# Performance work log

Measured on AMD Instinct MI355X. Metric: run time of the kernel, lower is better.

## Reference

```python
import jax, jax.numpy as jnp
import numpy as np

LN2 = float(np.log(2.0))
N_ATOMS = 100_000
N_PAIRS = 2_000_000
F = 64     # number_of_atom_features
R = 16     # number_of_radial_basis_functions
N_RES = 3


def setup_inputs() -> dict:
    key = jax.random.key(0)
    ks = jax.random.split(key, 16)
    s = 0.05
    inp = {
        "pair_indices": jax.random.randint(ks[0], (2, N_PAIRS), 0, N_ATOMS, dtype=jnp.int32),
        "f_ij": jax.random.normal(ks[1], (N_PAIRS, 1, R), dtype=jnp.float32),
        "d_ij": jax.random.uniform(ks[2], (N_PAIRS, 1), dtype=jnp.float32),
        "atomic_embedding": jax.random.normal(ks[3], (N_ATOMS, F), dtype=jnp.float32),
        # AttentionMask parameter G: [F, R]
        "G": jax.random.normal(ks[4], (F, R), dtype=jnp.float32),
        # interaction_i / interaction_j linear layers (stored as [in, out])
        "Wi": jax.random.normal(ks[5], (F, F), dtype=jnp.float32) * s,
        "bi": jnp.zeros((F,), dtype=jnp.float32),
        "Wj": jax.random.normal(ks[6], (F, F), dtype=jnp.float32) * s,
        "bj": jnp.zeros((F,), dtype=jnp.float32),
        # residual blocks, stacked over N_RES
        "res_W1": jax.random.normal(ks[7], (N_RES, F, F), dtype=jnp.float32) * s,
        "res_b1": jnp.zeros((N_RES, F), dtype=jnp.float32),
        "res_W2": jax.random.normal(ks[8], (N_RES, F, F), dtype=jnp.float32) * s,
        "res_b2": jnp.zeros((N_RES, F), dtype=jnp.float32),
        # process_v linear
        "Wv": jax.random.normal(ks[9], (F, F), dtype=jnp.float32) * s,
        "bv": jnp.zeros((F,), dtype=jnp.float32),
    }
    return inp


def reference(pair_indices, f_ij, d_ij, atomic_embedding,
              G, Wi, bi, Wj, bj, res_W1, res_b1, res_W2, res_b2, Wv, bv):
    idx_i, idx_j = pair_indices[0], pair_indices[1]
    f = f_ij.squeeze(1)                                  # [P, R]

    # ShiftedSoftplus on node embeddings
    x = jax.nn.softplus(atomic_embedding) - LN2          # [N, F]

    x_i_prime = jax.nn.softplus(x @ Wi + bi)             # [N, F]
    x_j_prime = jax.nn.softplus(x[idx_j] @ Wj + bj)      # [P, F] (gather)
    f_prime = f @ G.T                                    # [P, F] attention mask

    msg = x_j_prime * f_prime                            # [P, F]
    summed = jax.ops.segment_sum(msg, idx_i, num_segments=atomic_embedding.shape[0])

    v = x_i_prime + summed                               # [N, F]
    for l in range(res_W1.shape[0]):
        h = jax.nn.softplus(v @ res_W1[l] + res_b1[l])
        v = v + (h @ res_W2[l] + res_b2[l])
    return jax.nn.softplus(v) @ Wv + bv
```

## Files before the change

kernel.cpp:

```cpp
#include <hip/hip_runtime.h>
#include <math.h>

#define FDIM 64
#define RDIM 16
#define LN2F 0.69314718055994530942f
#define LTS 68

typedef __bf16 bf8_t __attribute__((ext_vector_type(8)));
typedef float  f4_t  __attribute__((ext_vector_type(4)));

__device__ __forceinline__ float sp(float x) {
    return fmaxf(x, 0.0f) + __logf(1.0f + __expf(-fabsf(x)));
}

__global__ __launch_bounds__(256) void k_prep(
    const float* s0, const float* s1, const float* s2, const float* s3,
    const float* s4, const float* s5, const float* s6, const float* s7,
    const float* s8, __bf16* __restrict__ dst)
{
    const float* srcs[9] = {s0, s1, s2, s3, s4, s5, s6, s7, s8};
    const float* W = srcs[blockIdx.x];
    __bf16* d = dst + (size_t)blockIdx.x * 4096;
    for (int slot = threadIdx.x; slot < 512; slot += 256) {
        int f = slot >> 6, l = slot & 63;
        int kt = f >> 2, nt = f & 3;
        int row0 = kt * 32 + (l >> 4) * 8;
        int col = nt * 16 + (l & 15);
#pragma unroll
        for (int j = 0; j < 8; ++j)
            d[slot * 8 + j] = (__bf16)W[(row0 + j) * FDIM + col];
    }
}

__global__ __launch_bounds__(256) void k_hist(
    const int* __restrict__ idx_i, int* __restrict__ cnt, int P)
{
    int t = blockIdx.x * blockDim.x + threadIdx.x;
    int n = gridDim.x * blockDim.x;
    for (int p = t; p < P; p += n) atomicAdd(&cnt[idx_i[p]], 1);
}

__device__ __forceinline__ void tile_in(float* T, const float* __restrict__ src,
                                        int a0, int rows, int lane)
{
#pragma unroll 4
    for (int i = 0; i < 16; ++i) {
        int r = i * 4 + (lane >> 4);
        int col = (lane & 15) * 4;
        float4 val = make_float4(0.f, 0.f, 0.f, 0.f);
        if (r < rows) val = *(const float4*)&src[(size_t)(a0 + r) * FDIM + col];
        *(float4*)&T[r * LTS + col] = val;
    }
}

__device__ __forceinline__ void build_a(const float* T, int lane, bool actLn2,
                                        bf8_t (&aF)[4][2])
{
    const int l15 = lane & 15, quad = lane >> 4;
#pragma unroll
    for (int mt = 0; mt < 4; ++mt) {
#pragma unroll
        for (int kt = 0; kt < 2; ++kt) {
            const float* rp = &T[(mt * 16 + l15) * LTS + kt * 32 + quad * 8];
            float4 u0 = *(const float4*)rp;
            float4 u1 = *(const float4*)(rp + 4);
            float e[8] = {u0.x, u0.y, u0.z, u0.w, u1.x, u1.y, u1.z, u1.w};
            bf8_t f;
#pragma unroll
            for (int j = 0; j < 8; ++j) {
                float t = actLn2 ? (sp(e[j]) - LN2F) : e[j];
                f[j] = (__bf16)t;
            }
            aF[mt][kt] = f;
        }
    }
}

__global__ __launch_bounds__(256) void k_atoms(
    const float* __restrict__ emb, const __bf16* __restrict__ wf,
    const float* __restrict__ bi, const float* __restrict__ bj,
    float* __restrict__ v, float* __restrict__ y, int N)
{
    __shared__ float tile[4][64 * LTS];
    const int lane = threadIdx.x & 63;
    const int wv = threadIdx.x >> 6;
    float* T = tile[wv];
    const int l15 = lane & 15, quad = lane >> 4;

    const bf8_t* wiF = (const bf8_t*)wf;
    const bf8_t* wjF = (const bf8_t*)(wf + 4096);
    bf8_t wi[2][4], wj[2][4];
#pragma unroll
    for (int kt = 0; kt < 2; ++kt)
#pragma unroll
        for (int nt = 0; nt < 4; ++nt) {
            wi[kt][nt] = wiF[(kt * 4 + nt) * 64 + lane];
            wj[kt][nt] = wjF[(kt * 4 + nt) * 64 + lane];
        }
    float biv[4], bjv[4];
#pragma unroll
    for (int nt = 0; nt < 4; ++nt) {
        biv[nt] = bi[nt * 16 + l15];
        bjv[nt] = bj[nt * 16 + l15];
    }

    const int nTiles = (N + 63) >> 6;
    for (int t = blockIdx.x * 4 + wv; t < nTiles; t += gridDim.x * 4) {
        const int a0 = t << 6;
        const int rows = min(64, N - a0);
        tile_in(T, emb, a0, rows, lane);
        bf8_t aF[4][2];
        build_a(T, lane, true, aF);
#pragma unroll
        for (int mt = 0; mt < 4; ++mt)
#pragma unroll
            for (int nt = 0; nt < 4; ++nt) {
                f4_t acc = {biv[nt], biv[nt], biv[nt], biv[nt]};
                acc = __builtin_amdgcn_mfma_f32_16x16x32_bf16(aF[mt][0], wi[0][nt], acc, 0, 0, 0);
                acc = __builtin_amdgcn_mfma_f32_16x16x32_bf16(aF[mt][1], wi[1][nt], acc, 0, 0, 0);
#pragma unroll
                for (int reg = 0; reg < 4; ++reg) {
                    int r = mt * 16 + quad * 4 + reg;
                    if (r < rows) v[(size_t)(a0 + r) * FDIM + nt * 16 + l15] = sp(acc[reg]);
                }
            }
#pragma unroll
        for (int mt = 0; mt < 4; ++mt)
#pragma unroll
            for (int nt = 0; nt < 4; ++nt) {
                f4_t acc = {bjv[nt], bjv[nt], bjv[nt], bjv[nt]};
                acc = __builtin_amdgcn_mfma_f32_16x16x32_bf16(aF[mt][0], wj[0][nt], acc, 0, 0, 0);
                acc = __builtin_amdgcn_mfma_f32_16x16x32_bf16(aF[mt][1], wj[1][nt], acc, 0, 0, 0);
#pragma unroll
                for (int reg = 0; reg < 4; ++reg) {
                    int r = mt * 16 + quad * 4 + reg;
                    if (r < rows) y[(size_t)(a0 + r) * FDIM + nt * 16 + l15] = sp(acc[reg]);
                }
            }
    }
}

__global__ __launch_bounds__(256) void k_post(
    const __bf16* __restrict__ wf,
    const float* __restrict__ rb1, const float* __restrict__ rb2,
    const float* __restrict__ bv,
    float* __restrict__ v, int N)
{
    __shared__ float tile[4][64 * LTS];
    const int lane = threadIdx.x & 63;
    const int wv = threadIdx.x >> 6;
    float* T = tile[wv];
    const int l15 = lane & 15, quad = lane >> 4;

    float b1v[3][4], b2v[3][4], bvv[4];
#pragma unroll
    for (int l = 0; l < 3; ++l)
#pragma unroll
        for (int nt = 0; nt < 4; ++nt) {
            b1v[l][nt] = rb1[l * FDIM + nt * 16 + l15];
            b2v[l][nt] = rb2[l * FDIM + nt * 16 + l15];
        }
#pragma unroll
    for (int nt = 0; nt < 4; ++nt) bvv[nt] = bv[nt * 16 + l15];

    const int nTiles = (N + 63) >> 6;
    for (int t = blockIdx.x * 4 + wv; t < nTiles; t += gridDim.x * 4) {
        const int a0 = t << 6;
        const int rows = min(64, N - a0);
        tile_in(T, v, a0, rows, lane);
        float vC[16][4];
#pragma unroll
        for (int mt = 0; mt < 4; ++mt)
#pragma unroll
            for (int nt = 0; nt < 4; ++nt)
#pragma unroll
                for (int reg = 0; reg < 4; ++reg)
                    vC[mt * 4 + nt][reg] =
                        T[(mt * 16 + quad * 4 + reg) * LTS + nt * 16 + l15];

        for (int l = 0; l < 3; ++l) {
            const bf8_t* w1f = (const bf8_t*)(wf + (size_t)(2 * l) * 4096);
            const bf8_t* w2f = (const bf8_t*)(wf + (size_t)(2 * l + 1) * 4096);
            bf8_t aF[4][2];
            build_a(T, lane, false, aF);
#pragma unroll
            for (int mt = 0; mt < 4; ++mt)
#pragma unroll
                for (int nt = 0; nt < 4; ++nt) {
                    f4_t acc = {b1v[l][nt], b1v[l][nt], b1v[l][nt], b1v[l][nt]};
                    acc = __builtin_amdgcn_mfma_f32_16x16x32_bf16(aF[mt][0], w1f[(0 * 4 + nt) * 64 + lane], acc, 0, 0, 0);
                    acc = __builtin_amdgcn_mfma_f32_16x16x32_bf16(aF[mt][1], w1f[(1 * 4 + nt) * 64 + lane], acc, 0, 0, 0);
#pragma unroll
                    for (int reg = 0; reg < 4; ++reg)
                        T[(mt * 16 + quad * 4 + reg) * LTS + nt * 16 + l15] = sp(acc[reg]);
                }
            bf8_t hF[4][2];
            build_a(T, lane, false, hF);
#pragma unroll
            for (int mt = 0; mt < 4; ++mt)
#pragma unroll
                for (int nt = 0; nt < 4; ++nt) {
                    f4_t acc = {b2v[l][nt], b2v[l][nt], b2v[l][nt], b2v[l][nt]};
                    acc = __builtin_amdgcn_mfma_f32_16x16x32_bf16(hF[mt][0], w2f[(0 * 4 + nt) * 64 + lane], acc, 0, 0, 0);
                    acc = __builtin_amdgcn_mfma_f32_16x16x32_bf16(hF[mt][1], w2f[(1 * 4 + nt) * 64 + lane], acc, 0, 0, 0);
#pragma unroll
                    for (int reg = 0; reg < 4; ++reg)
                        vC[mt * 4 + nt][reg] += acc[reg];
                }
            if (l < 2) {
#pragma unroll
                for (int mt = 0; mt < 4; ++mt)
#pragma unroll
                    for (int nt = 0; nt < 4; ++nt)
#pragma unroll
                        for (int reg = 0; reg < 4; ++reg)
                            T[(mt * 16 + quad * 4 + reg) * LTS + nt * 16 + l15] =
                                vC[mt * 4 + nt][reg];
            }
        }
#pragma unroll
        for (int mt = 0; mt < 4; ++mt)
#pragma unroll
            for (int nt = 0; nt < 4; ++nt)
#pragma unroll
                for (int reg = 0; reg < 4; ++reg)
                    T[(mt * 16 + quad * 4 + reg) * LTS + nt * 16 + l15] =
                        sp(vC[mt * 4 + nt][reg]);
        bf8_t fF[4][2];
        build_a(T, lane, false, fF);
        const bf8_t* wvf = (const bf8_t*)(wf + (size_t)6 * 4096);
#pragma unroll
        for (int mt = 0; mt < 4; ++mt)
#pragma unroll
            for (int nt = 0; nt < 4; ++nt) {
                f4_t acc = {bvv[nt], bvv[nt], bvv[nt], bvv[nt]};
                acc = __builtin_amdgcn_mfma_f32_16x16x32_bf16(fF[mt][0], wvf[(0 * 4 + nt) * 64 + lane], acc, 0, 0, 0);
                acc = __builtin_amdgcn_mfma_f32_16x16x32_bf16(fF[mt][1], wvf[(1 * 4 + nt) * 64 + lane], acc, 0, 0, 0);
#pragma unroll
                for (int reg = 0; reg < 4; ++reg) {
                    int r = mt * 16 + quad * 4 + reg;
                    if (r < rows) v[(size_t)(a0 + r) * FDIM + nt * 16 + l15] = acc[reg];
                }
            }
    }
}

__global__ __launch_bounds__(256) void k_scan_a(
    const int* __restrict__ cnt, int* __restrict__ part, int N)
{
    __shared__ int red[256];
    int b = blockIdx.x, t = threadIdx.x;
    int base = b * 1024 + t * 4;
    int s = 0;
#pragma unroll
    for (int i = 0; i < 4; ++i) { int a = base + i; if (a < N) s += cnt[a]; }
    red[t] = s; __syncthreads();
    for (int off = 128; off > 0; off >>= 1) {
        if (t < off) red[t] += red[t + off];
        __syncthreads();
    }
    if (t == 0) part[b] = red[0];
}

__global__ __launch_bounds__(256) void k_scan_b(int* __restrict__ part, int nPart)
{
    __shared__ int lds[256];
    int t = threadIdx.x;
    int base = t * 4;
    int v[4]; int s = 0;
#pragma unroll
    for (int i = 0; i < 4; ++i) { v[i] = (base + i < nPart) ? part[base + i] : 0; s += v[i]; }
    lds[t] = s; __syncthreads();
    int run = s;
    for (int off = 1; off < 256; off <<= 1) {
        int x = (t >= off) ? lds[t - off] : 0;
        __syncthreads();
        lds[t] += x;
        __syncthreads();
    }
    int excl = lds[t] - run;
#pragma unroll
    for (int i = 0; i < 4; ++i) { if (base + i < nPart) { part[base + i] = excl; excl += v[i]; } }
}

__global__ __launch_bounds__(256) void k_scan_c(
    const int* __restrict__ cnt, const int* __restrict__ part,
    int* __restrict__ start, int* __restrict__ cursor, int N, int P)
{
    __shared__ int lds[256];
    int b = blockIdx.x, t = threadIdx.x;
    int base = b * 1024 + t * 4;
    int v[4]; int s = 0;
#pragma unroll
    for (int i = 0; i < 4; ++i) { int a = base + i; v[i] = (a < N) ? cnt[a] : 0; s += v[i]; }
    lds[t] = s; __syncthreads();
    int run = s;
    for (int off = 1; off < 256; off <<= 1) {
        int x = (t >= off) ? lds[t - off] : 0;
        __syncthreads();
        lds[t] += x;
        __syncthreads();
    }
    int pre = part[b] + (lds[t] - run);
#pragma unroll
    for (int i = 0; i < 4; ++i) {
        int a = base + i;
        if (a < N) { start[a] = pre; cursor[a] = pre; pre += v[i]; }
    }
    if (b == 0 && t == 0) start[N] = P;
}

__global__ __launch_bounds__(256) void k_scatter(
    const int* __restrict__ pidx, int* __restrict__ cursor,
    int2* __restrict__ sorted, int P)
{
    int t = blockIdx.x * blockDim.x + threadIdx.x;
    int n = gridDim.x * blockDim.x;
    for (int p = t; p < P; p += n) {
        int i = pidx[p], j = pidx[P + p];
        int pos = atomicAdd(&cursor[i], 1);
        sorted[pos] = make_int2(p, j);
    }
}

__global__ __launch_bounds__(256) void k_seg(
    const int2* __restrict__ sorted, const int* __restrict__ start,
    const float* __restrict__ f_ij, const float* __restrict__ G,
    const float* __restrict__ y, float* __restrict__ v, int N)
{
    const int c = threadIdx.x & 63;
    const int w = __builtin_amdgcn_readfirstlane((blockIdx.x << 2) | (threadIdx.x >> 6));
    const int nw = gridDim.x << 2;

    float g[16];
    {
        const float4* gp = (const float4*)(G + c * RDIM);
        float4 g0 = gp[0], g1 = gp[1], g2 = gp[2], g3 = gp[3];
        g[0] = g0.x;  g[1] = g0.y;  g[2] = g0.z;  g[3] = g0.w;
        g[4] = g1.x;  g[5] = g1.y;  g[6] = g1.z;  g[7] = g1.w;
        g[8] = g2.x;  g[9] = g2.y;  g[10] = g2.z; g[11] = g2.w;
        g[12] = g3.x; g[13] = g3.y; g[14] = g3.z; g[15] = g3.w;
    }

    for (int a = w; a < N; a += nw) {
        const int s = start[a], e = start[a + 1];
        float vold = v[(size_t)a * FDIM + c];
        float t[16];
#pragma unroll
        for (int r = 0; r < 16; ++r) t[r] = 0.0f;

        for (int base = s; base < e; base += 64) {
            const int nn = (e - base < 64) ? (e - base) : 64;
            const int li = (c < nn) ? c : (nn - 1);
            const int2 E = sorted[base + li];
            const int pk = E.x, jk = E.y;

            int k = 0;
            for (; k + 4 <= nn; k += 4) {
                const int p0 = __builtin_amdgcn_readlane(pk, k + 0);
                const int j0 = __builtin_amdgcn_readlane(jk, k + 0);
                const int p1 = __builtin_amdgcn_readlane(pk, k + 1);
                const int j1 = __builtin_amdgcn_readlane(jk, k + 1);
                const int p2 = __builtin_amdgcn_readlane(pk, k + 2);
                const int j2 = __builtin_amdgcn_readlane(jk, k + 2);
                const int p3 = __builtin_amdgcn_readlane(pk, k + 3);
                const int j3 = __builtin_amdgcn_readlane(jk, k + 3);
                float y0 = y[(size_t)j0 * FDIM + c];
                float y1 = y[(size_t)j1 * FDIM + c];
                float y2 = y[(size_t)j2 * FDIM + c];
                float y3 = y[(size_t)j3 * FDIM + c];
                const float* f0 = f_ij + (size_t)p0 * RDIM;
                const float* f1 = f_ij + (size_t)p1 * RDIM;
                const float* f2 = f_ij + (size_t)p2 * RDIM;
                const float* f3 = f_ij + (size_t)p3 * RDIM;
#pragma unroll
                for (int r = 0; r < 16; ++r) t[r] = fmaf(f0[r], y0, t[r]);
#pragma unroll
                for (int r = 0; r < 16; ++r) t[r] = fmaf(f1[r], y1, t[r]);
#pragma unroll
                for (int r = 0; r < 16; ++r) t[r] = fmaf(f2[r], y2, t[r]);
#pragma unroll
                for (int r = 0; r < 16; ++r) t[r] = fmaf(f3[r], y3, t[r]);
            }
            for (; k < nn; ++k) {
                const int p0 = __builtin_amdgcn_readlane(pk, k);
                const int j0 = __builtin_amdgcn_readlane(jk, k);
                float y0 = y[(size_t)j0 * FDIM + c];
                const float* f0 = f_ij + (size_t)p0 * RDIM;
#pragma unroll
                for (int r = 0; r < 16; ++r) t[r] = fmaf(f0[r], y0, t[r]);
            }
        }

        float acc0 = 0.f, acc1 = 0.f, acc2 = 0.f, acc3 = 0.f;
#pragma unroll
        for (int r = 0; r < 16; r += 4) {
            acc0 = fmaf(g[r + 0], t[r + 0], acc0);
            acc1 = fmaf(g[r + 1], t[r + 1], acc1);
            acc2 = fmaf(g[r + 2], t[r + 2], acc2);
            acc3 = fmaf(g[r + 3], t[r + 3], acc3);
        }
        v[(size_t)a * FDIM + c] = vold + (acc0 + acc1) + (acc2 + acc3);
    }
}

extern "C" void kernel_launch(void* const* d_in, const int* in_sizes, int n_in,
                              void* d_out, int out_size, void* d_ws, size_t ws_size,
                              hipStream_t stream)
{
    const int*   pidx = (const int*)d_in[0];
    const float* f_ij = (const float*)d_in[1];
    const float* emb  = (const float*)d_in[3];
    const float* G    = (const float*)d_in[4];
    const float* Wi   = (const float*)d_in[5];
    const float* bi   = (const float*)d_in[6];
    const float* Wj   = (const float*)d_in[7];
    const float* bj   = (const float*)d_in[8];
    const float* rW1  = (const float*)d_in[9];
    const float* rb1  = (const float*)d_in[10];
    const float* rW2  = (const float*)d_in[11];
    const float* rb2  = (const float*)d_in[12];
    const float* Wv   = (const float*)d_in[13];
    const float* bv   = (const float*)d_in[14];

    const int P = in_sizes[0] / 2;
    const int N = in_sizes[3] / FDIM;

    float* v = (float*)d_out;

    char* ws = (char*)d_ws;
    size_t off = 0;
    float*  y      = (float*)(ws + off);  off += (size_t)N * FDIM * 4;
    int*    cnt    = (int*)(ws + off);    off += (size_t)N * 4;
    int*    start  = (int*)(ws + off);    off += (size_t)(N + 1) * 4;
    int*    cursor = (int*)(ws + off);    off += (size_t)N * 4;
    off = (off + 15) & ~(size_t)15;
    int*    part   = (int*)(ws + off);    off += (size_t)4096 * 4;
    off = (off + 15) & ~(size_t)15;
    int2*   sorted = (int2*)(ws + off);   off += (size_t)P * 8;
    off = (off + 15) & ~(size_t)15;
    __bf16* wf     = (__bf16*)(ws + off); off += (size_t)9 * 4096 * 2;

    const int nPart = (N + 1023) / 1024;
    const int nTiles = (N + 63) >> 6;
    const int gTiles = (nTiles + 3) / 4;

    dim3 blk(256);
    hipMemsetAsync(cnt, 0, (size_t)N * 4, stream);
    k_prep<<<9, blk, 0, stream>>>(Wi, Wj, rW1, rW2, rW1 + 4096, rW2 + 4096,
                                  rW1 + 8192, rW2 + 8192, Wv, wf);
    k_hist<<<1024, blk, 0, stream>>>(pidx, cnt, P);
    k_atoms<<<gTiles, blk, 0, stream>>>(emb, wf, bi, bj, v, y, N);
    k_scan_a<<<nPart, blk, 0, stream>>>(cnt, part, N);
    k_scan_b<<<1, blk, 0, stream>>>(part, nPart);
    k_scan_c<<<nPart, blk, 0, stream>>>(cnt, part, start, cursor, N, P);
    k_scatter<<<2048, blk, 0, stream>>>(pidx, cursor, sorted, P);
    k_seg<<<4096, blk, 0, stream>>>(sorted, start, f_ij, G, y, v, N);
    k_post<<<gTiles, blk, 0, stream>>>(wf + (size_t)2 * 4096, rb1, rb2, bv, v, N);
}
```

Baseline: 758.5 us.

## Pad per-atom counters to 64B lines and unroll atomics and gather loops

Counters and cursors are now stored one per 64-byte line (padding of 16 ints), and a single padded array serves first as the histogram and then as the scatter cursor. The aim is to stop atomics on neighbouring atoms from contending on the same cache line. The histogram and scatter loops are unrolled by four so more loads and atomics are in flight at once, and the histogram grid is doubled. The segment-sum inner loop gains an 8-way unrolled path that batches its gathers. In exchange, the counter array takes 16x more memory and its memset and the scan reads are strided, which costs extra bandwidth.

```diff
diff --git a/kernel.cpp b/kernel.cpp
--- a/kernel.cpp
+++ b/kernel.cpp
@@ -5,6 +5,7 @@
 #define RDIM 16
 #define LN2F 0.69314718055994530942f
 #define LTS 68
+#define CPAD 16
 
 typedef __bf16 bf8_t __attribute__((ext_vector_type(8)));
 typedef float  f4_t  __attribute__((ext_vector_type(4)));
@@ -33,11 +34,22 @@
 }
 
 __global__ __launch_bounds__(256) void k_hist(
-    const int* __restrict__ idx_i, int* __restrict__ cnt, int P)
+    const int* __restrict__ idx_i, int* __restrict__ cntP, int P)
 {
     int t = blockIdx.x * blockDim.x + threadIdx.x;
     int n = gridDim.x * blockDim.x;
-    for (int p = t; p < P; p += n) atomicAdd(&cnt[idx_i[p]], 1);
+    int p = t;
+    for (; p + 3 * n < P; p += 4 * n) {
+        int i0 = idx_i[p];
+        int i1 = idx_i[p + n];
+        int i2 = idx_i[p + 2 * n];
+        int i3 = idx_i[p + 3 * n];
+        atomicAdd(&cntP[(size_t)i0 * CPAD], 1);
+        atomicAdd(&cntP[(size_t)i1 * CPAD], 1);
+        atomicAdd(&cntP[(size_t)i2 * CPAD], 1);
+        atomicAdd(&cntP[(size_t)i3 * CPAD], 1);
+    }
+    for (; p < P; p += n) atomicAdd(&cntP[(size_t)idx_i[p] * CPAD], 1);
 }
 
 __device__ __forceinline__ void tile_in(float* T, const float* __restrict__ src,
@@ -246,14 +258,14 @@
 }
 
 __global__ __launch_bounds__(256) void k_scan_a(
-    const int* __restrict__ cnt, int* __restrict__ part, int N)
+    const int* __restrict__ cntP, int* __restrict__ part, int N)
 {
     __shared__ int red[256];
     int b = blockIdx.x, t = threadIdx.x;
     int base = b * 1024 + t * 4;
     int s = 0;
 #pragma unroll
-    for (int i = 0; i < 4; ++i) { int a = base + i; if (a < N) s += cnt[a]; }
+    for (int i = 0; i < 4; ++i) { int a = base + i; if (a < N) s += cntP[(size_t)a * CPAD]; }
     red[t] = s; __syncthreads();
     for (int off = 128; off > 0; off >>= 1) {
         if (t < off) red[t] += red[t + off];
@@ -284,15 +296,15 @@
 }
 
 __global__ __launch_bounds__(256) void k_scan_c(
-    const int* __restrict__ cnt, const int* __restrict__ part,
-    int* __restrict__ start, int* __restrict__ cursor, int N, int P)
+    const int* cntP, const int* __restrict__ part,
+    int* __restrict__ start, int* cursorP, int N, int P)
 {
     __shared__ int lds[256];
     int b = blockIdx.x, t = threadIdx.x;
     int base = b * 1024 + t * 4;
     int v[4]; int s = 0;
 #pragma unroll
-    for (int i = 0; i < 4; ++i) { int a = base + i; v[i] = (a < N) ? cnt[a] : 0; s += v[i]; }
+    for (int i = 0; i < 4; ++i) { int a = base + i; v[i] = (a < N) ? cntP[(size_t)a * CPAD] : 0; s += v[i]; }
     lds[t] = s; __syncthreads();
     int run = s;
     for (int off = 1; off < 256; off <<= 1) {
@@ -305,20 +317,35 @@
 #pragma unroll
     for (int i = 0; i < 4; ++i) {
         int a = base + i;
-        if (a < N) { start[a] = pre; cursor[a] = pre; pre += v[i]; }
+        if (a < N) { start[a] = pre; cursorP[(size_t)a * CPAD] = pre; pre += v[i]; }
     }
     if (b == 0 && t == 0) start[N] = P;
 }
 
 __global__ __launch_bounds__(256) void k_scatter(
-    const int* __restrict__ pidx, int* __restrict__ cursor,
+    const int* __restrict__ pidx, int* __restrict__ cursorP,
     int2* __restrict__ sorted, int P)
 {
     int t = blockIdx.x * blockDim.x + threadIdx.x;
     int n = gridDim.x * blockDim.x;
-    for (int p = t; p < P; p += n) {
+    int p = t;
+    for (; p + 3 * n < P; p += 4 * n) {
+        int i0 = pidx[p],         j0 = pidx[P + p];
+        int i1 = pidx[p + n],     j1 = pidx[P + p + n];
+        int i2 = pidx[p + 2 * n], j2 = pidx[P + p + 2 * n];
+        int i3 = pidx[p + 3 * n], j3 = pidx[P + p + 3 * n];
+        int q0 = atomicAdd(&cursorP[(size_t)i0 * CPAD], 1);
+        int q1 = atomicAdd(&cursorP[(size_t)i1 * CPAD], 1);
+        int q2 = atomicAdd(&cursorP[(size_t)i2 * CPAD], 1);
+        int q3 = atomicAdd(&cursorP[(size_t)i3 * CPAD], 1);
+        sorted[q0] = make_int2(p, j0);
+        sorted[q1] = make_int2(p + n, j1);
+        sorted[q2] = make_int2(p + 2 * n, j2);
+        sorted[q3] = make_int2(p + 3 * n, j3);
+    }
+    for (; p < P; p += n) {
         int i = pidx[p], j = pidx[P + p];
-        int pos = atomicAdd(&cursor[i], 1);
+        int pos = atomicAdd(&cursorP[(size_t)i * CPAD], 1);
         sorted[pos] = make_int2(p, j);
     }
 }
@@ -356,31 +383,41 @@
             const int pk = E.x, jk = E.y;
 
             int k = 0;
+            for (; k + 8 <= nn; k += 8) {
+                int pp[8], jj[8];
+#pragma unroll
+                for (int u = 0; u < 8; ++u) {
+                    pp[u] = __builtin_amdgcn_readlane(pk, k + u);
+                    jj[u] = __builtin_amdgcn_readlane(jk, k + u);
+                }
+                float yv[8];
+#pragma unroll
+                for (int u = 0; u < 8; ++u)
+                    yv[u] = y[(size_t)jj[u] * FDIM + c];
+#pragma unroll
+                for (int u = 0; u < 8; ++u) {
+                    const float* f = f_ij + (size_t)pp[u] * RDIM;
+#pragma unroll
+                    for (int r = 0; r < 16; ++r) t[r] = fmaf(f[r], yv[u], t[r]);
+                }
+            }
             for (; k + 4 <= nn; k += 4) {
-                const int p0 = __builtin_amdgcn_readlane(pk, k + 0);
-                const int j0 = __builtin_amdgcn_readlane(jk, k + 0);
-                const int p1 = __builtin_amdgcn_readlane(pk, k + 1);
-                const int j1 = __builtin_amdgcn_readlane(jk, k + 1);
-                const int p2 = __builtin_amdgcn_readlane(pk, k + 2);
-                const int j2 = __builtin_amdgcn_readlane(jk, k + 2);
-                const int p3 = __builtin_amdgcn_readlane(pk, k + 3);
-                const int j3 = __builtin_amdgcn_readlane(jk, k + 3);
-                float y0 = y[(size_t)j0 * FDIM + c];
-                float y1 = y[(size_t)j1 * FDIM + c];
-                float y2 = y[(size_t)j2 * FDIM + c];
-                float y3 = y[(size_t)j3 * FDIM + c];
-                const float* f0 = f_ij + (size_t)p0 * RDIM;
-                const float* f1 = f_ij + (size_t)p1 * RDIM;
-                const float* f2 = f_ij + (size_t)p2 * RDIM;
-                const float* f3 = f_ij + (size_t)p3 * RDIM;
-#pragma unroll
-                for (int r = 0; r < 16; ++r) t[r] = fmaf(f0[r], y0, t[r]);
-#pragma unroll
-                for (int r = 0; r < 16; ++r) t[r] = fmaf(f1[r], y1, t[r]);
-#pragma unroll
-                for (int r = 0; r < 16; ++r) t[r] = fmaf(f2[r], y2, t[r]);
-#pragma unroll
-                for (int r = 0; r < 16; ++r) t[r] = fmaf(f3[r], y3, t[r]);
+                int pp[4], jj[4];
+#pragma unroll
+                for (int u = 0; u < 4; ++u) {
+                    pp[u] = __builtin_amdgcn_readlane(pk, k + u);
+                    jj[u] = __builtin_amdgcn_readlane(jk, k + u);
+                }
+                float yv[4];
+#pragma unroll
+                for (int u = 0; u < 4; ++u)
+                    yv[u] = y[(size_t)jj[u] * FDIM + c];
+#pragma unroll
+                for (int u = 0; u < 4; ++u) {
+                    const float* f = f_ij + (size_t)pp[u] * RDIM;
+#pragma unroll
+                    for (int r = 0; r < 16; ++r) t[r] = fmaf(f[r], yv[u], t[r]);
+                }
             }
             for (; k < nn; ++k) {
                 const int p0 = __builtin_amdgcn_readlane(pk, k);
@@ -431,9 +468,8 @@
     char* ws = (char*)d_ws;
     size_t off = 0;
     float*  y      = (float*)(ws + off);  off += (size_t)N * FDIM * 4;
-    int*    cnt    = (int*)(ws + off);    off += (size_t)N * 4;
+    int*    cntP   = (int*)(ws + off);    off += (size_t)N * CPAD * 4;
     int*    start  = (int*)(ws + off);    off += (size_t)(N + 1) * 4;
-    int*    cursor = (int*)(ws + off);    off += (size_t)N * 4;
     off = (off + 15) & ~(size_t)15;
     int*    part   = (int*)(ws + off);    off += (size_t)4096 * 4;
     off = (off + 15) & ~(size_t)15;
@@ -446,15 +482,15 @@
     const int gTiles = (nTiles + 3) / 4;
 
     dim3 blk(256);
-    hipMemsetAsync(cnt, 0, (size_t)N * 4, stream);
+    hipMemsetAsync(cntP, 0, (size_t)N * CPAD * 4, stream);
     k_prep<<<9, blk, 0, stream>>>(Wi, Wj, rW1, rW2, rW1 + 4096, rW2 + 4096,
                                   rW1 + 8192, rW2 + 8192, Wv, wf);
-    k_hist<<<1024, blk, 0, stream>>>(pidx, cnt, P);
+    k_hist<<<2048, blk, 0, stream>>>(pidx, cntP, P);
     k_atoms<<<gTiles, blk, 0, stream>>>(emb, wf, bi, bj, v, y, N);
-    k_scan_a<<<nPart, blk, 0, stream>>>(cnt, part, N);
+    k_scan_a<<<nPart, blk, 0, stream>>>(cntP, part, N);
     k_scan_b<<<1, blk, 0, stream>>>(part, nPart);
-    k_scan_c<<<nPart, blk, 0, stream>>>(cnt, part, start, cursor, N, P);
-    k_scatter<<<2048, blk, 0, stream>>>(pidx, cursor, sorted, P);
+    k_scan_c<<<nPart, blk, 0, stream>>>(cntP, part, start, cntP, N, P);
+    k_scatter<<<2048, blk, 0, stream>>>(pidx, cntP, sorted, P);
     k_seg<<<4096, blk, 0, stream>>>(sorted, start, f_ij, G, y, v, N);
     k_post<<<gTiles, blk, 0, stream>>>(wf + (size_t)2 * 4096, rb1, rb2, bv, v, N);
 }
```

Result: no change. 768.6 us (+1.3%).
